# Optimization experiments

Hardware: AMD Instinct MI355X
Metric: run time of the kernel (lower is better)

## Reference

```python
import jax, jax.numpy as jnp
import numpy as np

H, DV, DM = 16, 64, 1024   # n_head, d_v, d_model
B, L = 8, 1024             # batch, seq len (len_k == len_v)
LN_EPS = 1e-5


def setup_inputs() -> dict:
    key = jax.random.key(0)
    ks = jax.random.split(key, 8)
    rn = lambda i, shape, scale=1.0: (jax.random.normal(ks[i], shape, jnp.float32) * scale)
    return {
        "q": rn(0, (B, L, DM)),
        "k": rn(1, (B, L, DM)),
        "v": rn(2, (B, L, DM)),
        "posi_att": rn(3, (H, L, L), 0.1),
        "w_k": rn(4, (H, DM), float(np.sqrt(2.0 / (DM + 1)))),
        "b_k": jnp.zeros((H,), jnp.float32),
        "w_v": rn(5, (H * DV, DM), float(np.sqrt(2.0 / (DM + DV)))),
        "b_v": jnp.zeros((H * DV,), jnp.float32),
        "w_fc": rn(6, (DM, H * DV), float(np.sqrt(2.0 / (DM + H * DV)))),
        "b_fc": jnp.zeros((DM,), jnp.float32),
        "ln_g": jnp.ones((DM,), jnp.float32),
        "ln_b": jnp.zeros((DM,), jnp.float32),
    }


def reference(q, k, v, posi_att, w_k, b_k, w_v, b_v, w_fc, b_fc, ln_g, ln_b):
    # q is unused by the original forward (only its device is read)
    b, l, _ = k.shape
    # key projection: d_k == 1, so one scalar per (token, head)
    kk = k @ w_k.T + b_k                               # [b, l, H]
    vv = (v @ w_v.T + b_v).reshape(b, l, H, DV)        # [b, l, H, DV]
    # temperature = sqrt(d_k) = 1.0 -> no-op, kept for faithfulness
    kk = kk / 1.0
    # scores[h, b, i, j] = kk[b, i, h] + posi_att[h, i, j]  (head-major, matches torch view)
    scores = kk.transpose(2, 0, 1)[..., None] + posi_att[:, None, :, :]  # [H, b, l, l]
    diag = jnp.eye(l, dtype=bool)
    scores = jnp.where(diag, -jnp.inf, scores)
    attn = jax.nn.softmax(scores, axis=-1)             # [H, b, l, l]
    # dropout is identity in eval mode
    out = jnp.einsum('hbqk,bkhd->bqhd', attn, vv).reshape(b, l, H * DV)
    out = out @ w_fc.T + b_fc                          # [b, l, DM]
    mu = out.mean(-1, keepdims=True)
    var = out.var(-1, keepdims=True)
    out = (out - mu) / jnp.sqrt(var + LN_EPS) * ln_g + ln_b
    return out, attn.reshape(H * b, l, l)
```

## Files before the change

kernel.cpp:

```cpp
#include <hip/hip_runtime.h>
#include <stdint.h>

#define NH 16
#define NDV 64
#define NDM 1024
#define NB 8
#define NL 1024

typedef __attribute__((ext_vector_type(8))) short short8;
typedef __attribute__((ext_vector_type(4))) short short4v;
typedef __attribute__((ext_vector_type(4))) float f32x4;

static __device__ __forceinline__ unsigned short f2bf(float x) {
    unsigned int u = __builtin_bit_cast(unsigned int, x);
    unsigned int r = (u + 0x7fffu + ((u >> 16) & 1u)) >> 16;
    return (unsigned short)r;
}

static __device__ __forceinline__ float waveMax(float v) {
#pragma unroll
    for (int o = 32; o > 0; o >>= 1) v = fmaxf(v, __shfl_xor(v, o, 64));
    return v;
}
static __device__ __forceinline__ float waveSum(float v) {
#pragma unroll
    for (int o = 32; o > 0; o >>= 1) v += __shfl_xor(v, o, 64);
    return v;
}

static __device__ __forceinline__ void gload_lds16(const void* g, void* l) {
    __builtin_amdgcn_global_load_lds((const __attribute__((address_space(1))) void*)g,
                                     (__attribute__((address_space(3))) void*)l, 16, 0, 0);
}

__global__ __launch_bounds__(256) void phaseA(
    const float* __restrict__ posi, float* __restrict__ attn_out,
    unsigned short* __restrict__ a_bf,
    const float* __restrict__ v, const float* __restrict__ wv, const float* __restrict__ wfc,
    unsigned short* __restrict__ v_bf, unsigned short* __restrict__ wv_bf,
    unsigned short* __restrict__ wfc_bf) {
    __shared__ float red[8];
    const int bid = blockIdx.x;
    const int t = threadIdx.x;
    if (bid < 16384) {
        const int h = bid >> 10, i = bid & 1023;
        const float4* rowp = (const float4*)(posi + (((size_t)h << 10) + i) * 1024);
        float4 p = rowp[t];
        const int j0 = t << 2;
        float* pf = (float*)&p;
        if (i >= j0 && i < j0 + 4) pf[i - j0] = -1e30f;
        float m = fmaxf(fmaxf(pf[0], pf[1]), fmaxf(pf[2], pf[3]));
        m = waveMax(m);
        if ((t & 63) == 0) red[t >> 6] = m;
        __syncthreads();
        m = fmaxf(fmaxf(red[0], red[1]), fmaxf(red[2], red[3]));
        const float e0 = __expf(pf[0] - m), e1 = __expf(pf[1] - m);
        const float e2 = __expf(pf[2] - m), e3 = __expf(pf[3] - m);
        float s = waveSum(e0 + e1 + e2 + e3);
        if ((t & 63) == 0) red[4 + (t >> 6)] = s;
        __syncthreads();
        s = red[4] + red[5] + red[6] + red[7];
        const float inv = 1.0f / s;
        float4 a;
        a.x = e0 * inv; a.y = e1 * inv; a.z = e2 * inv; a.w = e3 * inv;
        float* base = attn_out + (((size_t)(h << 3)) << 20) + ((size_t)i << 10);
#pragma unroll
        for (int b = 0; b < 8; ++b)
            ((float4*)(base + ((size_t)b << 20)))[t] = a;
        short4v u;
        u[0] = (short)f2bf(a.x); u[1] = (short)f2bf(a.y);
        u[2] = (short)f2bf(a.z); u[3] = (short)f2bf(a.w);
        *(short4v*)(a_bf + ((((size_t)h << 10) + i) << 10) + j0) = u;
    } else {
        int b = bid - 16384;
        const float* src;
        unsigned short* dst;
        if (b < 8192)      { src = v;   dst = v_bf; }
        else if (b < 9216) { src = wv;  dst = wv_bf;  b -= 8192; }
        else               { src = wfc; dst = wfc_bf; b -= 9216; }
        const size_t idx = ((size_t)b * 256 + t) << 2;
        const float4 x = *(const float4*)(src + idx);
        short4v u;
        u[0] = (short)f2bf(x.x); u[1] = (short)f2bf(x.y);
        u[2] = (short)f2bf(x.z); u[3] = (short)f2bf(x.w);
        *(short4v*)(dst + idx) = u;
    }
}

template <int EPI>
static __device__ __forceinline__ void gemm128_core(
    const unsigned short* __restrict__ A,
    const unsigned short* __restrict__ Bt,
    const float* __restrict__ bias,
    void* __restrict__ Cout,
    const int K, const int tm, const int tn, const int bh,
    unsigned short* sA, unsigned short* sB) {
    const int tid = threadIdx.x;
    const int lane = tid & 63;
    const int w = tid >> 6;
    const int wr = w >> 1, wc = w & 1;

    const unsigned short* Ab = A + (size_t)tm * 128 * K;
    const unsigned short* Bb = Bt + (size_t)tn * 128 * K;

    const int r0 = w * 32 + (lane >> 2);
    const int ch = lane & 3;
    const int so = ((ch ^ ((r0 >> 1) & 3)) << 3);
    const unsigned short* gA0 = Ab + (size_t)r0 * K + so;
    const unsigned short* gA1 = Ab + (size_t)(r0 + 16) * K + so;
    const unsigned short* gB0 = Bb + (size_t)r0 * K + so;
    const unsigned short* gB1 = Bb + (size_t)(r0 + 16) * K + so;
    const int ldsOff = w * 1024;

    const int c = lane >> 4;
    int offA[4], offB[4];
#pragma unroll
    for (int f = 0; f < 4; ++f) {
        const int fra = wr * 64 + f * 16 + (lane & 15);
        offA[f] = fra * 32 + ((c ^ ((fra >> 1) & 3)) << 3);
        const int frb = wc * 64 + f * 16 + (lane & 15);
        offB[f] = frb * 32 + ((c ^ ((frb >> 1) & 3)) << 3);
    }

    f32x4 acc[4][4];
#pragma unroll
    for (int i = 0; i < 4; ++i)
#pragma unroll
        for (int j = 0; j < 4; ++j) acc[i][j] = (f32x4){0.f, 0.f, 0.f, 0.f};

    const int nst = K >> 5;
    {
        unsigned short* lA = sA + ldsOff;
        unsigned short* lB = sB + ldsOff;
        gload_lds16(gA0, lA);
        gload_lds16(gA1, lA + 512);
        gload_lds16(gB0, lB);
        gload_lds16(gB1, lB + 512);
    }
    __syncthreads();

    int cur = 0;
    for (int t = 0; t < nst; ++t) {
        if (t + 1 < nst) {
            const int kt = (t + 1) << 5;
            unsigned short* lA = sA + ((cur ^ 1) << 12) + ldsOff;
            unsigned short* lB = sB + ((cur ^ 1) << 12) + ldsOff;
            gload_lds16(gA0 + kt, lA);
            gload_lds16(gA1 + kt, lA + 512);
            gload_lds16(gB0 + kt, lB);
            gload_lds16(gB1 + kt, lB + 512);
        }
        const unsigned short* bA = sA + (cur << 12);
        const unsigned short* bB = sB + (cur << 12);
        short8 af[4], bfv[4];
#pragma unroll
        for (int f = 0; f < 4; ++f) af[f] = *(const short8*)&bA[offA[f]];
#pragma unroll
        for (int f = 0; f < 4; ++f) bfv[f] = *(const short8*)&bB[offB[f]];
        __builtin_amdgcn_s_setprio(1);
#pragma unroll
        for (int i = 0; i < 4; ++i)
#pragma unroll
            for (int j = 0; j < 4; ++j)
                acc[i][j] = __builtin_amdgcn_mfma_f32_16x16x32_bf16(af[i], bfv[j], acc[i][j], 0, 0, 0);
        __builtin_amdgcn_s_setprio(0);
        if (t + 1 < nst) __syncthreads();
        cur ^= 1;
    }

#pragma unroll
    for (int i = 0; i < 4; ++i) {
        const int gRow0 = tm * 128 + wr * 64 + i * 16 + ((lane >> 4) << 2);
#pragma unroll
        for (int j = 0; j < 4; ++j) {
            const int gCol = tn * 128 + wc * 64 + j * 16 + (lane & 15);
            f32x4 v = acc[i][j];
            if (EPI == 1) {
                const float bb2 = bias[gCol];
                const int hh = gCol >> 6, dd = gCol & 63;
                const int b = gRow0 >> 10, ll2 = gRow0 & 1023;
                unsigned short* C = (unsigned short*)Cout;
                short4v u;
                u[0] = (short)f2bf(v[0] + bb2);
                u[1] = (short)f2bf(v[1] + bb2);
                u[2] = (short)f2bf(v[2] + bb2);
                u[3] = (short)f2bf(v[3] + bb2);
                *(short4v*)(C + (size_t)hh * 524288 + ((size_t)b * 64 + dd) * 1024 + ll2) = u;
            } else if (EPI == 2) {
                const int b = gCol >> 6, dd = gCol & 63;
                unsigned short* X = (unsigned short*)Cout;
#pragma unroll
                for (int r = 0; r < 4; ++r)
                    X[((size_t)b * 1024 + gRow0 + r) * 1024 + bh * 64 + dd] = f2bf(v[r]);
            } else {
                const float bb2 = bias[gCol];
                float* O = (float*)Cout;
#pragma unroll
                for (int r = 0; r < 4; ++r)
                    O[(size_t)(gRow0 + r) * 1024 + gCol] = v[r] + bb2;
            }
        }
    }
}

__global__ __launch_bounds__(256) void gemm_k1(const unsigned short* __restrict__ A,
                                               const unsigned short* __restrict__ Bt,
                                               const float* __restrict__ bias,
                                               unsigned short* __restrict__ C) {
    __shared__ unsigned short sA[8192], sB[8192];
    const int s = (blockIdx.x & 7) * 64 + (blockIdx.x >> 3);
    gemm128_core<1>(A, Bt, bias, C, 1024, s >> 3, s & 7, 0, sA, sB);
}

__global__ __launch_bounds__(256) void gemm_k2(const unsigned short* __restrict__ A,
                                               const unsigned short* __restrict__ Bt,
                                               unsigned short* __restrict__ X) {
    __shared__ unsigned short sA[8192], sB[8192];
    const int s = (blockIdx.x & 7) * 64 + (blockIdx.x >> 3);
    const int bh = s >> 5;
    gemm128_core<2>(A + (size_t)bh * 1048576, Bt + (size_t)bh * 524288, nullptr, X,
                    1024, (s >> 2) & 7, s & 3, bh, sA, sB);
}

__global__ __launch_bounds__(256) void gemm_k3(const unsigned short* __restrict__ A,
                                               const unsigned short* __restrict__ Bt,
                                               const float* __restrict__ bias,
                                               float* __restrict__ O) {
    __shared__ unsigned short sA[8192], sB[8192];
    const int s = (blockIdx.x & 7) * 64 + (blockIdx.x >> 3);
    gemm128_core<3>(A, Bt, bias, O, 1024, s >> 3, s & 7, 0, sA, sB);
}

__global__ __launch_bounds__(256) void ln_kernel(float* __restrict__ out,
                                                 const float* __restrict__ g,
                                                 const float* __restrict__ b) {
    __shared__ float red[8];
    const int row = blockIdx.x, t = threadIdx.x;
    float4* p = (float4*)(out + ((size_t)row << 10));
    float4 x = p[t];
    float s = x.x + x.y + x.z + x.w;
    float sq = x.x * x.x + x.y * x.y + x.z * x.z + x.w * x.w;
    s = waveSum(s);
    sq = waveSum(sq);
    if ((t & 63) == 0) { red[t >> 6] = s; red[4 + (t >> 6)] = sq; }
    __syncthreads();
    s = red[0] + red[1] + red[2] + red[3];
    sq = red[4] + red[5] + red[6] + red[7];
    const float mu = s * (1.f / 1024.f);
    const float var = sq * (1.f / 1024.f) - mu * mu;
    const float rinv = rsqrtf(var + 1e-5f);
    const float4 gg = ((const float4*)g)[t];
    const float4 bb = ((const float4*)b)[t];
    x.x = (x.x - mu) * rinv * gg.x + bb.x;
    x.y = (x.y - mu) * rinv * gg.y + bb.y;
    x.z = (x.z - mu) * rinv * gg.z + bb.z;
    x.w = (x.w - mu) * rinv * gg.w + bb.w;
    p[t] = x;
}

extern "C" void kernel_launch(void* const* d_in, const int* in_sizes, int n_in,
                              void* d_out, int out_size, void* d_ws, size_t ws_size,
                              hipStream_t stream) {
    const float* v    = (const float*)d_in[2];
    const float* posi = (const float*)d_in[3];
    const float* w_v  = (const float*)d_in[6];
    const float* b_v  = (const float*)d_in[7];
    const float* w_fc = (const float*)d_in[8];
    const float* b_fc = (const float*)d_in[9];
    const float* ln_g = (const float*)d_in[10];
    const float* ln_b = (const float*)d_in[11];

    float* out = (float*)d_out;
    float* attn_out = out + (size_t)NB * NL * NDM;

    char* ws = (char*)d_ws;
    unsigned short* A_bf   = (unsigned short*)(ws);
    unsigned short* v_bf   = (unsigned short*)(ws + 33554432);
    unsigned short* wv_bf  = (unsigned short*)(ws + 50331648);
    unsigned short* wfc_bf = (unsigned short*)(ws + 52428800);
    unsigned short* vvT    = (unsigned short*)(ws + 54525952);
    unsigned short* X      = (unsigned short*)(ws + 71303168);

    phaseA<<<26624, 256, 0, stream>>>(posi, attn_out, A_bf, v, w_v, w_fc, v_bf, wv_bf, wfc_bf);
    gemm_k1<<<512, 256, 0, stream>>>(v_bf, wv_bf, b_v, vvT);
    gemm_k2<<<512, 256, 0, stream>>>(A_bf, vvT, X);
    gemm_k3<<<512, 256, 0, stream>>>(X, wfc_bf, b_fc, out);
    ln_kernel<<<8192, 256, 0, stream>>>(out, ln_g, ln_b);
}
```

Before: 252.2 us.

## Triple-buffer GEMM LDS tiles with vmcnt-based waits and single barrier

Turns the shared GEMM core's double-buffered LDS pipeline into a three-stage ring. Two k-tiles are prefetched up front, and each iteration waits only on the older group of async global-to-LDS loads (vmcnt(4)) before a single barrier. The aim is more global-load latency in flight and one fewer barrier per k-step. In exchange, LDS per block grows from 32KB to 48KB, which may lower occupancy, and the manual waitcnt depends on exact load counts.

```diff
diff --git a/kernel.cpp b/kernel.cpp
--- a/kernel.cpp
+++ b/kernel.cpp
@@ -129,22 +129,32 @@
         for (int j = 0; j < 4; ++j) acc[i][j] = (f32x4){0.f, 0.f, 0.f, 0.f};
 
     const int nst = K >> 5;
-    {
-        unsigned short* lA = sA + ldsOff;
-        unsigned short* lB = sB + ldsOff;
-        gload_lds16(gA0, lA);
-        gload_lds16(gA1, lA + 512);
-        gload_lds16(gB0, lB);
-        gload_lds16(gB1, lB + 512);
-    }
-    __syncthreads();
+
+#pragma unroll
+    for (int p = 0; p < 2; ++p) {
+        unsigned short* lA = sA + (p << 12) + ldsOff;
+        unsigned short* lB = sB + (p << 12) + ldsOff;
+        const int kt = p << 5;
+        gload_lds16(gA0 + kt, lA);
+        gload_lds16(gA1 + kt, lA + 512);
+        gload_lds16(gB0 + kt, lB);
+        gload_lds16(gB1 + kt, lB + 512);
+    }
 
     int cur = 0;
     for (int t = 0; t < nst; ++t) {
         if (t + 1 < nst) {
-            const int kt = (t + 1) << 5;
-            unsigned short* lA = sA + ((cur ^ 1) << 12) + ldsOff;
-            unsigned short* lB = sB + ((cur ^ 1) << 12) + ldsOff;
+            asm volatile("s_waitcnt vmcnt(4)" ::: "memory");
+        } else {
+            asm volatile("s_waitcnt vmcnt(0)" ::: "memory");
+        }
+        __builtin_amdgcn_s_barrier();
+        __builtin_amdgcn_sched_barrier(0);
+        if (t + 2 < nst) {
+            const int sb = (cur + 2 >= 3) ? cur - 1 : cur + 2;
+            unsigned short* lA = sA + (sb << 12) + ldsOff;
+            unsigned short* lB = sB + (sb << 12) + ldsOff;
+            const int kt = (t + 2) << 5;
             gload_lds16(gA0 + kt, lA);
             gload_lds16(gA1 + kt, lA + 512);
             gload_lds16(gB0 + kt, lB);
@@ -164,8 +174,7 @@
             for (int j = 0; j < 4; ++j)
                 acc[i][j] = __builtin_amdgcn_mfma_f32_16x16x32_bf16(af[i], bfv[j], acc[i][j], 0, 0, 0);
         __builtin_amdgcn_s_setprio(0);
-        if (t + 1 < nst) __syncthreads();
-        cur ^= 1;
+        cur = (cur == 2) ? 0 : cur + 1;
     }
 
 #pragma unroll
@@ -207,7 +216,7 @@
                                                const unsigned short* __restrict__ Bt,
                                                const float* __restrict__ bias,
                                                unsigned short* __restrict__ C) {
-    __shared__ unsigned short sA[8192], sB[8192];
+    __shared__ unsigned short sA[12288], sB[12288];
     const int s = (blockIdx.x & 7) * 64 + (blockIdx.x >> 3);
     gemm128_core<1>(A, Bt, bias, C, 1024, s >> 3, s & 7, 0, sA, sB);
 }
@@ -215,7 +224,7 @@
 __global__ __launch_bounds__(256) void gemm_k2(const unsigned short* __restrict__ A,
                                                const unsigned short* __restrict__ Bt,
                                                unsigned short* __restrict__ X) {
-    __shared__ unsigned short sA[8192], sB[8192];
+    __shared__ unsigned short sA[12288], sB[12288];
     const int s = (blockIdx.x & 7) * 64 + (blockIdx.x >> 3);
     const int bh = s >> 5;
     gemm128_core<2>(A + (size_t)bh * 1048576, Bt + (size_t)bh * 524288, nullptr, X,
@@ -226,7 +235,7 @@
                                                const unsigned short* __restrict__ Bt,
                                                const float* __restrict__ bias,
                                                float* __restrict__ O) {
-    __shared__ unsigned short sA[8192], sB[8192];
+    __shared__ unsigned short sA[12288], sB[12288];
     const int s = (blockIdx.x & 7) * 64 + (blockIdx.x >> 3);
     gemm128_core<3>(A, Bt, bias, O, 1024, s >> 3, s & 7, 0, sA, sB);
 }
```

New measurement: 248.5 us. Within noise of the previous version (-1.5%).
